# Kernel tuning notes

Hardware: AMD Instinct MI355X
Metric: run time of the kernel (lower is better)

Reference implementation:

```python
import jax, jax.numpy as jnp
import numpy as np

BINS = 100
VMIN = 0.0
VMAX = 1.0
DELTA = (VMAX - VMIN) / BINS
EPS = 1e-5


def setup_inputs() -> dict:
    key = jax.random.key(0)
    x = jax.random.uniform(key, (32, 1048576), dtype=jnp.float32)  # [B, N] pixel values in [0,1]
    return {"x": x}


def reference(x):
    # bin centers: min + delta*(i + 0.5)
    centers = VMIN + DELTA * (jnp.arange(BINS, dtype=x.dtype) + 0.5)  # [bins]
    # Triangular-kernel soft count per bin: relu(delta - |x - c|) summed over N.
    # lax.map over the small fixed bin set keeps peak memory at one [B, N]
    # intermediate instead of materializing [bins, B, N].
    counts = jax.lax.map(
        lambda c: jnp.maximum(DELTA - jnp.abs(x - c), 0.0).sum(axis=1),
        centers,
    )  # [bins, B]
    out = counts.T  # [B, bins]
    # norm=True: divide each row by its sum (+eps)
    summ = out.sum(axis=1) + EPS  # [B]
    return out / summ[:, None]
```

## Files before the change

### kernel.cpp

```cpp
#include <hip/hip_runtime.h>


#define BINS 100
#define ROWS 101
#define BATCH 32
#define NPER 1048576
#define TPB 256
#define WAVES 4
#define COLS 32
#define BPR 24
#define GRID (BATCH * BPR)
#define NF4_ROW (NPER / 4)
#define STRIDE (BPR * TPB)
#define HCELLS (WAVES * ROWS * COLS)

typedef float f32x4 __attribute__((ext_vector_type(4)));

__global__ __launch_bounds__(TPB, 3) void hist_kernel(const float* __restrict__ x,
                                                      float* __restrict__ partial) {
    __shared__ uint32_t h[HCELLS];
    const int tid = threadIdx.x;

    uint4* h4 = reinterpret_cast<uint4*>(h);
    for (int i = tid; i < HCELLS / 4; i += TPB) h4[i] = make_uint4(0, 0, 0, 0);
    __syncthreads();

    const int row  = blockIdx.x / BPR;
    const int jblk = blockIdx.x % BPR;
    const int wave = tid >> 6;
    const int col  = (tid & 63) >> 1;
    uint32_t* hw = h + wave * (ROWS * COLS) + col;

    const f32x4* src = reinterpret_cast<const f32x4*>(x + (size_t)row * NPER);
    for (int i = jblk * TPB + tid; i < NF4_ROW; i += STRIDE) {
        f32x4 v = src[i];
#pragma unroll
        for (int e = 0; e < 4; ++e) {
            float U = __builtin_fmaf(v[e], 25600.0f, 128.0f);
            int  iU = (int)U;
            int   r = iU >> 8;
            uint32_t inc = 0x10000u | (uint32_t)(iU & 255);
            atomicAdd(&hw[r * COLS], inc);
        }
    }
    __syncthreads();

    uint32_t s0 = 0, s1 = 0;
    const int a0 = tid, a1 = tid + TPB;
    {
        int w = a0 / ROWS, r = a0 - w * ROWS;
        const uint32_t* base = h + w * (ROWS * COLS) + r * COLS;
        uint32_t s = 0;
#pragma unroll
        for (int c = 0; c < COLS; ++c) s += base[(c + tid) & (COLS - 1)];
        s0 = s;
    }
    if (a1 < WAVES * ROWS) {
        int w = a1 / ROWS, r = a1 - w * ROWS;
        const uint32_t* base = h + w * (ROWS * COLS) + r * COLS;
        uint32_t s = 0;
#pragma unroll
        for (int c = 0; c < COLS; ++c) s += base[(c + tid) & (COLS - 1)];
        s1 = s;
    }
    __syncthreads();
    h[a0] = s0 >> 16;
    h[512 + a0] = s0 & 0xFFFFu;
    if (a1 < WAVES * ROWS) { h[a1] = s1 >> 16; h[512 + a1] = s1 & 0xFFFFu; }
    __syncthreads();
    if (tid < ROWS) {
        uint32_t N = h[tid] + h[101 + tid] + h[202 + tid] + h[303 + tid];
        uint32_t W = h[512 + tid] + h[613 + tid] + h[714 + tid] + h[815 + tid];
        h[1024 + tid] = N;
        h[1536 + tid] = W;
    }
    __syncthreads();
    if (tid < BINS) {
        float N1 = (float)h[1024 + tid + 1];
        float W1 = (float)h[1536 + tid + 1];
        float W0 = (float)h[1536 + tid];
        partial[blockIdx.x * BINS + tid] = N1 + (W0 - W1) * (1.0f / 256.0f);
    }
}

__global__ __launch_bounds__(128) void norm_kernel(const float* __restrict__ partial,
                                                   float* __restrict__ out) {
    __shared__ float sarr[2];
    const int row = blockIdx.x;
    const int t   = threadIdx.x;
    float cnt = 0.0f;
    if (t < BINS) {
        const float* p = partial + (size_t)row * BPR * BINS + t;
#pragma unroll
        for (int j = 0; j < BPR; ++j) cnt += p[j * BINS];
    }
    float s = cnt;
#pragma unroll
    for (int off = 32; off > 0; off >>= 1) s += __shfl_down(s, off);
    if ((t & 63) == 0) sarr[t >> 6] = s;
    __syncthreads();
    const float total = sarr[0] + sarr[1];
    if (t < BINS) {
        out[row * BINS + t] = 0.01f * cnt / (0.01f * total + 1e-5f);
    }
}

extern "C" void kernel_launch(void* const* d_in, const int* in_sizes, int n_in,
                              void* d_out, int out_size, void* d_ws, size_t ws_size,
                              hipStream_t stream) {
    const float* x = (const float*)d_in[0];
    float* out = (float*)d_out;
    float* partial = (float*)d_ws;

    hist_kernel<<<GRID, TPB, 0, stream>>>(x, partial);
    norm_kernel<<<BATCH, 128, 0, stream>>>(partial, out);
}
```

Measured before the change: 31.28 us.

## Fuse histogram and normalization via cooperative launch with grid sync

The histogram kernel and the normalization kernel are merged into one cooperative kernel. A grid-wide barrier separates them, after which the first BATCH blocks sum the per-block partials and write the normalized output. This removes the second kernel launch and its gap. In exchange it adds the cost of a grid sync and requires all 768 blocks to be co-resident, falling back to the two-kernel path if the cooperative launch fails.

```diff
diff --git a/kernel.cpp b/kernel.cpp
--- a/kernel.cpp
+++ b/kernel.cpp
@@ -1,4 +1,7 @@
 #include <hip/hip_runtime.h>
+#include <hip/hip_cooperative_groups.h>
+
+namespace cg = cooperative_groups;
 
 
 #define BINS 100
@@ -16,8 +19,10 @@
 
 typedef float f32x4 __attribute__((ext_vector_type(4)));
 
-__global__ __launch_bounds__(TPB, 3) void hist_kernel(const float* __restrict__ x,
-                                                      float* __restrict__ partial) {
+template <int FUSED>
+__device__ __forceinline__ void hist_body(const float* __restrict__ x,
+                                          float* __restrict__ partial,
+                                          float* __restrict__ out) {
     __shared__ uint32_t h[HCELLS];
     const int tid = threadIdx.x;
 
@@ -81,6 +86,44 @@
         float W0 = (float)h[1536 + tid];
         partial[blockIdx.x * BINS + tid] = N1 + (W0 - W1) * (1.0f / 256.0f);
     }
+
+    if constexpr (FUSED) {
+        cg::this_grid().sync();
+        if (blockIdx.x < BATCH) {
+            const int nrow = blockIdx.x;
+            float* csum = reinterpret_cast<float*>(h);
+            float cnt = 0.0f;
+            if (tid < BINS) {
+                const float* p = partial + (size_t)nrow * BPR * BINS + tid;
+#pragma unroll
+                for (int j = 0; j < BPR; ++j) cnt += p[j * BINS];
+                csum[tid] = cnt;
+            }
+            __syncthreads();
+            if (tid < 64) {
+                float s = csum[tid] + ((tid + 64 < BINS) ? csum[tid + 64] : 0.0f);
+#pragma unroll
+                for (int off = 32; off > 0; off >>= 1) s += __shfl_down(s, off);
+                if (tid == 0) csum[BINS] = s;
+            }
+            __syncthreads();
+            const float total = csum[BINS];
+            if (tid < BINS)
+                out[nrow * BINS + tid] = 0.01f * cnt / (0.01f * total + 1e-5f);
+        }
+    }
+}
+
+__global__ __launch_bounds__(TPB, 3) void hist_fused(const float* __restrict__ x,
+                                                     float* __restrict__ partial,
+                                                     float* __restrict__ out) {
+    hist_body<1>(x, partial, out);
+}
+
+__global__ __launch_bounds__(TPB, 3) void hist_plain(const float* __restrict__ x,
+                                                     float* __restrict__ partial,
+                                                     float* __restrict__ out) {
+    hist_body<0>(x, partial, out);
 }
 
 __global__ __launch_bounds__(128) void norm_kernel(const float* __restrict__ partial,
@@ -112,6 +155,12 @@
     float* out = (float*)d_out;
     float* partial = (float*)d_ws;
 
-    hist_kernel<<<GRID, TPB, 0, stream>>>(x, partial);
-    norm_kernel<<<BATCH, 128, 0, stream>>>(partial, out);
+    void* args[] = {(void*)&x, (void*)&partial, (void*)&out};
+    hipError_t e = hipLaunchCooperativeKernel((const void*)hist_fused,
+                                              dim3(GRID), dim3(TPB),
+                                              args, 0, stream);
+    if (e != hipSuccess) {
+        hist_plain<<<GRID, TPB, 0, stream>>>(x, partial, out);
+        norm_kernel<<<BATCH, 128, 0, stream>>>(partial, out);
+    }
 }
```

After: 110.6 us. 254% more time.
